# Kernel optimization log

Hardware: AMD Instinct MI355X
Metric: run time of the kernel (lower is better)

The kernel has to match this reference:

```python
import jax, jax.numpy as jnp
import numpy as np

N, E, IN, HID, H, G, CLS = 20000, 160000, 128, 96, 6, 512, 128
HD = H * HID  # heads * out_channels = 576
ARC_S = 30.0  # ArcFace scale (no margin at inference, no labels passed)


def _lin_params(key, fan_in, fan_out):
    k1, k2 = jax.random.split(key)
    lim = 1.0 / np.sqrt(fan_in)
    W = jax.random.uniform(k1, (fan_in, fan_out), minval=-lim, maxval=lim, dtype=jnp.float32)
    b = jax.random.uniform(k2, (fan_out,), minval=-lim, maxval=lim, dtype=jnp.float32)
    return W, b


def setup_inputs() -> dict:
    key = jax.random.key(0)
    ks = jax.random.split(key, 32)
    x = jax.random.normal(ks[0], (N, IN), dtype=jnp.float32)
    edge_index = jax.random.randint(ks[1], (2, E), 0, N, dtype=jnp.int64)
    batch = jnp.sort(jax.random.randint(ks[2], (N,), 0, G, dtype=jnp.int64))
    # conv1: IN -> HID (per-head dim HID, H heads)
    Wq1, bq1 = _lin_params(ks[3], IN, HD)
    Wk1, bk1 = _lin_params(ks[4], IN, HD)
    Wv1, bv1 = _lin_params(ks[5], IN, HD)
    Ws1, bs1 = _lin_params(ks[6], IN, HID)
    # convs 2..5 share shapes: HID -> HID, stacked on leading axis of 4
    def stack(fn_keys, fi, fo):
        Ws, bs = zip(*[_lin_params(k, fi, fo) for k in fn_keys])
        return jnp.stack(Ws), jnp.stack(bs)
    Wq_r, bq_r = stack(ks[7:11], HID, HD)
    Wk_r, bk_r = stack(ks[11:15], HID, HD)
    Wv_r, bv_r = stack(ks[15:19], HID, HD)
    Ws_r, bs_r = stack(ks[19:23], HID, HID)
    fc1_w, fc1_b = _lin_params(ks[23], HID, HID)
    fc2_w, fc2_b = _lin_params(ks[24], HID, HID)
    arc_w = jax.random.normal(ks[25], (CLS, HID), dtype=jnp.float32)
    return dict(x=x, edge_index=edge_index, batch=batch,
                Wq1=Wq1, bq1=bq1, Wk1=Wk1, bk1=bk1, Wv1=Wv1, bv1=bv1, Ws1=Ws1, bs1=bs1,
                Wq_r=Wq_r, bq_r=bq_r, Wk_r=Wk_r, bk_r=bk_r, Wv_r=Wv_r, bv_r=bv_r,
                Ws_r=Ws_r, bs_r=bs_r,
                fc1_w=fc1_w, fc1_b=fc1_b, fc2_w=fc2_w, fc2_b=fc2_b, arc_w=arc_w)


def transformer_conv(x, src, dst, Wq, bq, Wk, bk, Wv, bv, Ws, bs):
    n = x.shape[0]
    q = (x @ Wq + bq).reshape(n, H, HID)
    k = (x @ Wk + bk).reshape(n, H, HID)
    v = (x @ Wv + bv).reshape(n, H, HID)
    # edge-wise attention logits [E, H]
    alpha = jnp.einsum('ehd,ehd->eh', q[dst], k[src]) / jnp.sqrt(jnp.float32(HID))
    # segment softmax over incoming edges of each destination node
    m = jax.ops.segment_max(alpha, dst, num_segments=n)
    a = jnp.exp(alpha - m[dst])
    s = jax.ops.segment_sum(a, dst, num_segments=n)
    a = a / s[dst]
    out = jax.ops.segment_sum(a[:, :, None] * v[src], dst, num_segments=n)  # [n, H, HID]
    # concat=False -> mean over heads; root_weight skip connection
    return out.mean(axis=1) + x @ Ws + bs


def reference(x, edge_index, batch,
              Wq1, bq1, Wk1, bk1, Wv1, bv1, Ws1, bs1,
              Wq_r, bq_r, Wk_r, bk_r, Wv_r, bv_r, Ws_r, bs_r,
              fc1_w, fc1_b, fc2_w, fc2_b, arc_w):
    src, dst = edge_index[0], edge_index[1]
    h = jax.nn.relu(transformer_conv(x, src, dst, Wq1, bq1, Wk1, bk1, Wv1, bv1, Ws1, bs1))
    for i in range(4):  # gtconv2..gtconv5
        h = jax.nn.relu(transformer_conv(h, src, dst, Wq_r[i], bq_r[i], Wk_r[i], bk_r[i],
                                         Wv_r[i], bv_r[i], Ws_r[i], bs_r[i]))
    # global mean pool over graphs
    sums = jax.ops.segment_sum(h, batch, num_segments=G)
    cnt = jax.ops.segment_sum(jnp.ones((h.shape[0], 1), h.dtype), batch, num_segments=G)
    g = sums / jnp.maximum(cnt, 1.0)
    g = jax.nn.relu(g @ fc1_w + fc1_b)
    g = jax.nn.relu(g @ fc2_w + fc2_b)
    # ArcFace without labels: scaled cosine logits
    gn = g / (jnp.linalg.norm(g, axis=-1, keepdims=True) + 1e-12)
    wn = arc_w / (jnp.linalg.norm(arc_w, axis=-1, keepdims=True) + 1e-12)
    return ARC_S * (gn @ wn.T)
```

## Files before the change

kernel.cpp:

```cpp
#include <hip/hip_runtime.h>
#include <math.h>

#define N_NODES 20000
#define N_EDGES 160000
#define DIM_IN  128
#define HIDDEN  96
#define NH      6
#define HD      576
#define LDROW   704
#define KVF8LD  1152
#define NALL    1824
#define NGRAPH  512
#define NCLS    128
#define CHUNK   32
#define SLD     104
#define BSTR    112

typedef unsigned short ushort_t;
typedef unsigned char uchar_t;
typedef __attribute__((ext_vector_type(8))) short bf16x8;
typedef __attribute__((ext_vector_type(4))) float f32x4;
typedef __attribute__((ext_vector_type(2))) float f32x2;

static __device__ __forceinline__ ushort_t f2bf(float f) {
    unsigned int u = __float_as_uint(f);
    return (ushort_t)((u + 0x7fffu + ((u >> 16) & 1u)) >> 16);
}
static __device__ __forceinline__ float bfs(ushort_t u) { return __uint_as_float((unsigned int)u << 16); }
static __device__ __forceinline__ float bflo(unsigned int u) { return __uint_as_float(u << 16); }
static __device__ __forceinline__ float bfhi(unsigned int u) { return __uint_as_float(u & 0xffff0000u); }

__global__ void k_cvt(const float* __restrict__ src, ushort_t* __restrict__ dst, int n)
{
    int i = blockIdx.x * blockDim.x + threadIdx.x;
    if (i < n) dst[i] = f2bf(src[i]);
}

__global__ void k_cvt_wT_all(
    const float* __restrict__ Wq1, const float* __restrict__ Wk1,
    const float* __restrict__ Wv1, const float* __restrict__ Ws1,
    const float* __restrict__ Wq_r, const float* __restrict__ Wk_r,
    const float* __restrict__ Wv_r, const float* __restrict__ Ws_r,
    ushort_t* __restrict__ Wb0, ushort_t* __restrict__ Wbr)
{
    const int L = blockIdx.y;
    const int K = (L == 0) ? DIM_IN : HIDDEN;
    int i = blockIdx.x * blockDim.x + threadIdx.x;
    if (i >= K * NALL) return;
    const float *Wq, *Wk, *Wv, *Ws; ushort_t* dst;
    if (L == 0) { Wq = Wq1; Wk = Wk1; Wv = Wv1; Ws = Ws1; dst = Wb0; }
    else {
        int j = L - 1;
        Wq = Wq_r + (size_t)j * HIDDEN * HD; Wk = Wk_r + (size_t)j * HIDDEN * HD;
        Wv = Wv_r + (size_t)j * HIDDEN * HD; Ws = Ws_r + (size_t)j * HIDDEN * HIDDEN;
        dst = Wbr + (size_t)j * HIDDEN * NALL;
    }
    int n = i / K, k = i - n * K;
    float v;
    if (n < 576)       v = Wq[(size_t)k * HD + n];
    else if (n < 1152) v = Wk[(size_t)k * HD + (n - 576)];
    else if (n < 1728) v = Wv[(size_t)k * HD + (n - 1152)];
    else               v = Ws[(size_t)k * HIDDEN + (n - 1728)];
    dst[i] = f2bf(v);
}

template<int KDIM>
__global__ __launch_bounds__(256) void gemm_qkvs_mfma(
    const ushort_t* __restrict__ A, int M,
    const ushort_t* __restrict__ WbT,
    const float* __restrict__ bq, const float* __restrict__ bk,
    const float* __restrict__ bv, const float* __restrict__ bs,
    ushort_t* __restrict__ kvqs, uchar_t* __restrict__ kvf8)
{
    constexpr int LDB = KDIM + 8;
    constexpr int K8  = KDIM >> 3;
    __shared__ __align__(16) ushort_t smem[128 * SLD];
    const int t    = threadIdx.x;
    const int lane = t & 63;
    const int w    = t >> 6;
    const int wm   = w & 1, wn = w >> 1;
    const int quad = lane >> 4;
    const int l16  = lane & 15;
    const int m0   = blockIdx.y * 128;
    const int rb   = blockIdx.x;
    const int n0   = rb * 96;

    for (int idx = t; idx < 96 * K8; idx += 256) {
        int c = idx / K8, kc = idx - c * K8;
        uint4 v = *(const uint4*)(WbT + (size_t)(n0 + c) * KDIM + kc * 8);
        *(uint4*)(&smem[c * LDB + kc * 8]) = v;
    }

    const ushort_t* Arow[4];
    #pragma unroll
    for (int i = 0; i < 4; i++) {
        int row = m0 + wm * 64 + i * 16 + l16;
        row = min(row, M - 1);
        Arow[i] = A + (size_t)row * KDIM + quad * 8;
    }
    __syncthreads();

    f32x4 acc[4][3] = {};
    #pragma unroll
    for (int ks = 0; ks < KDIM; ks += 32) {
        bf16x8 af[4], bfv[3];
        #pragma unroll
        for (int i = 0; i < 4; i++) af[i] = *(const bf16x8*)(Arow[i] + ks);
        #pragma unroll
        for (int j = 0; j < 3; j++)
            bfv[j] = *(const bf16x8*)(&smem[(wn * 48 + j * 16 + l16) * LDB + ks + quad * 8]);
        #pragma unroll
        for (int i = 0; i < 4; i++)
            #pragma unroll
            for (int j = 0; j < 3; j++)
                acc[i][j] = __builtin_amdgcn_mfma_f32_16x16x32_bf16(af[i], bfv[j], acc[i][j], 0, 0, 0);
    }

    int region; const float* biasp;
    if (rb < 6)       { region = 0; biasp = bq; }
    else if (rb < 12) { region = 1; biasp = bk; }
    else if (rb < 18) { region = 2; biasp = bv; }
    else              { region = 3; biasp = bs; }
    const int colbase = (region == 3) ? 0 : (rb - region * 6) * 96;
    float bj[3];
    #pragma unroll
    for (int j = 0; j < 3; j++) bj[j] = biasp[colbase + wn * 48 + j * 16 + l16];

    __syncthreads();

    if (region == 1 || region == 2) {
        uchar_t* bstage = (uchar_t*)smem;
        #pragma unroll
        for (int i = 0; i < 4; i++) {
            #pragma unroll
            for (int r = 0; r < 4; r++) {
                int row = wm * 64 + i * 16 + quad * 4 + r;
                #pragma unroll
                for (int j = 0; j < 3; j++) {
                    float v = acc[i][j][r] + bj[j];
                    int pk = __builtin_amdgcn_cvt_pk_fp8_f32(v, v, 0, false);
                    bstage[row * BSTR + wn * 48 + j * 16 + l16] = (uchar_t)(pk & 0xff);
                }
            }
        }
        __syncthreads();
        const int c0 = (rb - 6) * 96;
        for (int idx = t; idx < 128 * 6; idx += 256) {
            int r = idx / 6, v4 = idx - r * 6;
            int row = m0 + r;
            if (row < M)
                *(uint4*)(kvf8 + (size_t)row * KVF8LD + c0 + v4 * 16) =
                    *(const uint4*)(bstage + r * BSTR + v4 * 16);
        }
    } else {
        int dstoff = (region == 0) ? n0 : 576;
        #pragma unroll
        for (int i = 0; i < 4; i++) {
            #pragma unroll
            for (int r = 0; r < 4; r++) {
                int row = wm * 64 + i * 16 + quad * 4 + r;
                #pragma unroll
                for (int j = 0; j < 3; j++)
                    smem[row * SLD + wn * 48 + j * 16 + l16] = f2bf(acc[i][j][r] + bj[j]);
            }
        }
        __syncthreads();
        for (int idx = t; idx < 128 * 12; idx += 256) {
            int r = idx / 12, v = idx - r * 12;
            int row = m0 + r;
            if (row < M)
                *(uint4*)(kvqs + (size_t)row * LDROW + dstoff + v * 8) =
                    *(const uint4*)(&smem[r * SLD + v * 8]);
        }
    }
}

__global__ void k_deg(const int* __restrict__ edst, int* __restrict__ deg)
{
    int e = blockIdx.x * blockDim.x + threadIdx.x;
    if (e < N_EDGES) atomicAdd(&deg[edst[e]], 1);
}

__global__ __launch_bounds__(1024) void k_scan(const int* __restrict__ deg,
                                               int* __restrict__ row_ptr,
                                               int* __restrict__ cursor)
{
    __shared__ int part[1024];
    int t = threadIdx.x;
    const int chunk = (N_NODES + 1023) / 1024;
    int b = t * chunk;
    int s = 0;
    for (int i = 0; i < chunk; i++)
        if (b + i < N_NODES) s += deg[b + i];
    part[t] = s;
    __syncthreads();
    for (int o = 1; o < 1024; o <<= 1) {
        int v = (t >= o) ? part[t - o] : 0;
        __syncthreads();
        part[t] += v;
        __syncthreads();
    }
    int run = part[t] - s;
    for (int i = 0; i < chunk; i++) {
        if (b + i < N_NODES) {
            row_ptr[b + i] = run;
            cursor[b + i]  = run;
            run += deg[b + i];
        }
    }
    if (t == 1023) row_ptr[N_NODES] = part[1023];
}

__global__ void k_scatter(const int* __restrict__ esrc, const int* __restrict__ edst,
                          int* __restrict__ cursor, int* __restrict__ csrc)
{
    int e = blockIdx.x * blockDim.x + threadIdx.x;
    if (e < N_EDGES) {
        int pos = atomicAdd(&cursor[edst[e]], 1);
        csrc[pos] = esrc[e];
    }
}

__global__ void k_gbound(const int* __restrict__ batch, int* __restrict__ gbound)
{
    int g = blockIdx.x * blockDim.x + threadIdx.x;
    if (g > NGRAPH) return;
    int lo = 0, hi = N_NODES;
    while (lo < hi) {
        int mid = (lo + hi) >> 1;
        if (batch[mid] < g) lo = mid + 1; else hi = mid;
    }
    gbound[g] = lo;
}

__global__ __launch_bounds__(192) void node_attn(
    const ushort_t* __restrict__ kvqs, const uchar_t* __restrict__ kvf8,
    const int* __restrict__ row_ptr, const int* __restrict__ csrc,
    ushort_t* __restrict__ hb, float* __restrict__ hf)
{
    const int n = blockIdx.x;
    const int t = threadIdx.x;
    const int lane = t & 31;
    const int g = t >> 5;
    const int el = lane >> 2;
    const int qr = lane & 3;

    __shared__ float Qs[HD];
    __shared__ float wbuf[CHUNK * NH];
    __shared__ int   srcs[CHUNK];
    __shared__ float m[NH], l[NH], scale[NH], linv[NH];
    __shared__ float arr[HD];

    const int beg = row_ptr[n], end = row_ptr[n + 1];
    const ushort_t* qk = kvqs + (size_t)n * LDROW;

    if (t < 72) {
        uint4 v = *(const uint4*)(qk + t * 8);
        unsigned int uu[4] = {v.x, v.y, v.z, v.w};
        #pragma unroll
        for (int j = 0; j < 4; j++) {
            Qs[t * 8 + 2 * j]     = bflo(uu[j]);
            Qs[t * 8 + 2 * j + 1] = bfhi(uu[j]);
        }
    }
    if (t < NH) { m[t] = -1e30f; l[t] = 0.f; }

    const int d4 = 4 * t;
    const int hh = d4 / HIDDEN;
    float a[4] = {0.f, 0.f, 0.f, 0.f};
    const float qa = 0.10206207261596577f;
    const uchar_t* vbase = kvf8 + 576 + d4;

    for (int cb = beg; cb < end; cb += CHUNK) {
        const int c = min(CHUNK, end - cb);
        __syncthreads();
        if (t < c) srcs[t] = csrc[cb + t];
        __syncthreads();

        for (int eb = 0; eb < c; eb += 8) {
            int e8 = eb + el;
            bool act = e8 < c;
            int src = srcs[act ? e8 : 0];
            const uchar_t* kp = kvf8 + (size_t)src * KVF8LD + g * HIDDEN + qr * 24;
            uint2 a0 = *(const uint2*)(kp);
            uint2 a1 = *(const uint2*)(kp + 8);
            uint2 a2 = *(const uint2*)(kp + 16);
            const float* qb = &Qs[g * HIDDEN + qr * 24];
            unsigned int uu[6] = {a0.x, a0.y, a1.x, a1.y, a2.x, a2.y};
            float p = 0.f;
            #pragma unroll
            for (int k2 = 0; k2 < 6; k2++) {
                f32x2 lo = __builtin_amdgcn_cvt_pk_f32_fp8(uu[k2], false);
                f32x2 hi = __builtin_amdgcn_cvt_pk_f32_fp8(uu[k2], true);
                p += lo[0] * qb[4 * k2]     + lo[1] * qb[4 * k2 + 1]
                   + hi[0] * qb[4 * k2 + 2] + hi[1] * qb[4 * k2 + 3];
            }
            p += __shfl_xor(p, 1, 32);
            p += __shfl_xor(p, 2, 32);
            if (act && qr == 0) wbuf[e8 * NH + g] = p * qa;
        }
        __syncthreads();

        {
            float logit = (lane < c) ? wbuf[lane * NH + g] : -1e30f;
            float cm = logit;
            #pragma unroll
            for (int o = 16; o; o >>= 1) cm = fmaxf(cm, __shfl_xor(cm, o, 32));
            cm = fmaxf(cm, m[g]);
            float wv = (lane < c) ? __expf(logit - cm) : 0.f;
            if (lane < c) wbuf[lane * NH + g] = wv;
            float lp = wv;
            #pragma unroll
            for (int o = 16; o; o >>= 1) lp += __shfl_xor(lp, o, 32);
            if (lane == 0) {
                float sc = __expf(m[g] - cm);
                scale[g] = sc;
                l[g] = l[g] * sc + lp;
                m[g] = cm;
            }
        }
        __syncthreads();

        if (t < 144) {
            float sc = scale[hh];
            #pragma unroll
            for (int j = 0; j < 4; j++) a[j] *= sc;
            int e = 0;
            for (; e + 4 <= c; e += 4) {
                unsigned int r[4];
                #pragma unroll
                for (int j = 0; j < 4; j++)
                    r[j] = *(const unsigned int*)(vbase + (size_t)srcs[e + j] * KVF8LD);
                #pragma unroll
                for (int j = 0; j < 4; j++) {
                    float w2 = wbuf[(e + j) * NH + hh];
                    f32x2 lo = __builtin_amdgcn_cvt_pk_f32_fp8(r[j], false);
                    f32x2 hi = __builtin_amdgcn_cvt_pk_f32_fp8(r[j], true);
                    a[0] += w2 * lo[0];
                    a[1] += w2 * lo[1];
                    a[2] += w2 * hi[0];
                    a[3] += w2 * hi[1];
                }
            }
            for (; e < c; e++) {
                unsigned int r = *(const unsigned int*)(vbase + (size_t)srcs[e] * KVF8LD);
                float w2 = wbuf[e * NH + hh];
                f32x2 lo = __builtin_amdgcn_cvt_pk_f32_fp8(r, false);
                f32x2 hi = __builtin_amdgcn_cvt_pk_f32_fp8(r, true);
                a[0] += w2 * lo[0];
                a[1] += w2 * lo[1];
                a[2] += w2 * hi[0];
                a[3] += w2 * hi[1];
            }
        }
    }

    if (t < NH) linv[t] = (l[t] > 0.f) ? 1.0f / l[t] : 0.f;
    __syncthreads();
    if (t < 144) {
        float li = linv[hh];
        #pragma unroll
        for (int j = 0; j < 4; j++) arr[d4 + j] = a[j] * li;
    }
    __syncthreads();

    if (t < HIDDEN) {
        float s = (arr[t] + arr[HIDDEN + t] + arr[2 * HIDDEN + t] +
                   arr[3 * HIDDEN + t] + arr[4 * HIDDEN + t] + arr[5 * HIDDEN + t])
                  * (1.0f / 6.0f);
        s += bfs(qk[576 + t]);
        s = fmaxf(s, 0.0f);
        hb[n * HIDDEN + t] = f2bf(s);
        hf[n * HIDDEN + t] = s;
    }
}

__global__ __launch_bounds__(128) void k_head(
    const float* __restrict__ hf, const int* __restrict__ gbound,
    const float* __restrict__ fc1w, const float* __restrict__ fc1b,
    const float* __restrict__ fc2w, const float* __restrict__ fc2b,
    const float* __restrict__ arcw, float* __restrict__ out)
{
    int g = blockIdx.x, t = threadIdx.x;
    __shared__ float v0[HIDDEN], v1[HIDDEN], v2[HIDDEN];
    __shared__ float gnorm;
    const int s0 = gbound[g], s1 = gbound[g + 1];
    float cnt = fmaxf((float)(s1 - s0), 1.0f);
    if (t < HIDDEN) {
        float s = 0.f;
        for (int n = s0; n < s1; n++) s += hf[(size_t)n * HIDDEN + t];
        v0[t] = s / cnt;
    }
    __syncthreads();
    if (t < HIDDEN) {
        float s = fc1b[t];
        for (int k = 0; k < HIDDEN; k++) s += v0[k] * fc1w[k * HIDDEN + t];
        v1[t] = fmaxf(s, 0.f);
    }
    __syncthreads();
    if (t < HIDDEN) {
        float s = fc2b[t];
        for (int k = 0; k < HIDDEN; k++) s += v1[k] * fc2w[k * HIDDEN + t];
        v2[t] = fmaxf(s, 0.f);
    }
    __syncthreads();
    if (t == 0) {
        float s = 0.f;
        for (int k = 0; k < HIDDEN; k++) s += v2[k] * v2[k];
        gnorm = sqrtf(s) + 1e-12f;
    }
    __syncthreads();
    if (t < NCLS) {
        float dot = 0.f, wn = 0.f;
        const float* wr = arcw + (size_t)t * HIDDEN;
        for (int k = 0; k < HIDDEN; k++) {
            float w = wr[k];
            dot += w * v2[k];
            wn  += w * w;
        }
        out[g * NCLS + t] = 30.0f * dot / (gnorm * (sqrtf(wn) + 1e-12f));
    }
}

extern "C" void kernel_launch(void* const* d_in, const int* in_sizes, int n_in,
                              void* d_out, int out_size, void* d_ws, size_t ws_size,
                              hipStream_t stream)
{
    (void)in_sizes; (void)n_in; (void)out_size; (void)ws_size;

    const float* x     = (const float*)d_in[0];
    const int*   ei    = (const int*)d_in[1];
    const int*   batch = (const int*)d_in[2];
    const float* Wq1 = (const float*)d_in[3];  const float* bq1 = (const float*)d_in[4];
    const float* Wk1 = (const float*)d_in[5];  const float* bk1 = (const float*)d_in[6];
    const float* Wv1 = (const float*)d_in[7];  const float* bv1 = (const float*)d_in[8];
    const float* Ws1 = (const float*)d_in[9];  const float* bs1 = (const float*)d_in[10];
    const float* Wq_r = (const float*)d_in[11]; const float* bq_r = (const float*)d_in[12];
    const float* Wk_r = (const float*)d_in[13]; const float* bk_r = (const float*)d_in[14];
    const float* Wv_r = (const float*)d_in[15]; const float* bv_r = (const float*)d_in[16];
    const float* Ws_r = (const float*)d_in[17]; const float* bs_r = (const float*)d_in[18];
    const float* fc1w = (const float*)d_in[19]; const float* fc1b = (const float*)d_in[20];
    const float* fc2w = (const float*)d_in[21]; const float* fc2b = (const float*)d_in[22];
    const float* arcw = (const float*)d_in[23];
    float* out = (float*)d_out;

    const int* esrc = ei;
    const int* edst = ei + N_EDGES;

    char* base = (char*)d_ws;
    size_t off = 0;
    auto alloc = [&](size_t bytes) -> void* {
        off = (off + 255) & ~(size_t)255;
        void* p = base + off;
        off += bytes;
        return p;
    };
    ushort_t* kvqs = (ushort_t*)alloc((size_t)N_NODES * LDROW * 2);
    uchar_t*  kvf8 = (uchar_t*)alloc((size_t)N_NODES * KVF8LD);
    ushort_t* xb  = (ushort_t*)alloc((size_t)N_NODES * DIM_IN * 2);
    ushort_t* hb0 = (ushort_t*)alloc((size_t)N_NODES * HIDDEN * 2);
    ushort_t* hb1 = (ushort_t*)alloc((size_t)N_NODES * HIDDEN * 2);
    float*    hf  = (float*)alloc((size_t)N_NODES * HIDDEN * 4);
    ushort_t* Wb0 = (ushort_t*)alloc((size_t)DIM_IN * NALL * 2);
    ushort_t* Wbr = (ushort_t*)alloc((size_t)4 * HIDDEN * NALL * 2);
    int*   deg     = (int*)alloc(N_NODES * 4);
    int*   row_ptr = (int*)alloc((N_NODES + 1) * 4);
    int*   cursor  = (int*)alloc(N_NODES * 4);
    int*   csrc    = (int*)alloc(N_EDGES * 4);
    int*   gbound  = (int*)alloc((NGRAPH + 1) * 4);

    k_cvt<<<(N_NODES * DIM_IN + 255) / 256, 256, 0, stream>>>(x, xb, N_NODES * DIM_IN);
    {
        dim3 gw((DIM_IN * NALL + 255) / 256, 5);
        k_cvt_wT_all<<<gw, 256, 0, stream>>>(Wq1, Wk1, Wv1, Ws1,
                                             Wq_r, Wk_r, Wv_r, Ws_r, Wb0, Wbr);
    }

    hipMemsetAsync(deg, 0, N_NODES * 4, stream);
    k_deg<<<(N_EDGES + 255) / 256, 256, 0, stream>>>(edst, deg);
    k_scan<<<1, 1024, 0, stream>>>(deg, row_ptr, cursor);
    k_scatter<<<(N_EDGES + 255) / 256, 256, 0, stream>>>(esrc, edst, cursor, csrc);
    k_gbound<<<(NGRAPH + 1 + 255) / 256, 256, 0, stream>>>(batch, gbound);

    const ushort_t* Ain = xb;
    ushort_t* hbcur = hb0;
    for (int L = 0; L < 5; L++) {
        const ushort_t* Wb = (L == 0) ? Wb0 : (Wbr + (size_t)(L - 1) * HIDDEN * NALL);
        const float *bq, *bk, *bv, *bs;
        if (L == 0) { bq = bq1; bk = bk1; bv = bv1; bs = bs1; }
        else {
            int i = L - 1;
            bq = bq_r + (size_t)i * HD; bk = bk_r + (size_t)i * HD;
            bv = bv_r + (size_t)i * HD; bs = bs_r + (size_t)i * HIDDEN;
        }
        dim3 g(19, (N_NODES + 127) / 128);
        if (L == 0)
            gemm_qkvs_mfma<DIM_IN><<<g, 256, 0, stream>>>(Ain, N_NODES, Wb,
                                                          bq, bk, bv, bs, kvqs, kvf8);
        else
            gemm_qkvs_mfma<HIDDEN><<<g, 256, 0, stream>>>(Ain, N_NODES, Wb,
                                                          bq, bk, bv, bs, kvqs, kvf8);
        node_attn<<<N_NODES, 192, 0, stream>>>(kvqs, kvf8, row_ptr, csrc, hbcur, hf);
        Ain = hbcur;
        hbcur = (hbcur == hb0) ? hb1 : hb0;
    }

    k_head<<<NGRAPH, 128, 0, stream>>>(hf, gbound, fc1w, fc1b, fc2w, fc2b, arcw, out);
}
```

Measured before the change: 530.7 us.

## Enlarge QKVS GEMM M-tile to 256 rows and merge prep kernels

The QKVS GEMM now has each warp cover 64 rows by all 96 columns, which doubles the block's M-tile to 256 rows and halves the grid. Each B fragment is reused across more rows, and the epilogue is written out in two halves through the same shared buffer. Separately, the x conversion, degree count and graph-boundary search are merged into one launch to cut launch overhead. The cost is twice the accumulator registers per thread, which may lower occupancy, and fewer blocks across the GPU.

```diff
diff --git a/kernel.cpp b/kernel.cpp
--- a/kernel.cpp
+++ b/kernel.cpp
@@ -30,10 +30,31 @@
 static __device__ __forceinline__ float bflo(unsigned int u) { return __uint_as_float(u << 16); }
 static __device__ __forceinline__ float bfhi(unsigned int u) { return __uint_as_float(u & 0xffff0000u); }
 
-__global__ void k_cvt(const float* __restrict__ src, ushort_t* __restrict__ dst, int n)
-{
-    int i = blockIdx.x * blockDim.x + threadIdx.x;
-    if (i < n) dst[i] = f2bf(src[i]);
+#define PREP_CVT_BLOCKS 10000
+#define PREP_DEG_BLOCKS 625
+#define PREP_GB_BLOCKS  3
+__global__ void k_prep(const float* __restrict__ x, ushort_t* __restrict__ xb,
+                       const int* __restrict__ edst, int* __restrict__ deg,
+                       const int* __restrict__ batch, int* __restrict__ gbound)
+{
+    int b = blockIdx.x;
+    if (b < PREP_CVT_BLOCKS) {
+        int i = b * 256 + threadIdx.x;
+        if (i < N_NODES * DIM_IN) xb[i] = f2bf(x[i]);
+    } else if (b < PREP_CVT_BLOCKS + PREP_DEG_BLOCKS) {
+        int e = (b - PREP_CVT_BLOCKS) * 256 + threadIdx.x;
+        if (e < N_EDGES) atomicAdd(&deg[edst[e]], 1);
+    } else {
+        int g = (b - PREP_CVT_BLOCKS - PREP_DEG_BLOCKS) * 256 + threadIdx.x;
+        if (g <= NGRAPH) {
+            int lo = 0, hi = N_NODES;
+            while (lo < hi) {
+                int mid = (lo + hi) >> 1;
+                if (batch[mid] < g) lo = mid + 1; else hi = mid;
+            }
+            gbound[g] = lo;
+        }
+    }
 }
 
 __global__ void k_cvt_wT_all(
@@ -78,10 +99,9 @@
     const int t    = threadIdx.x;
     const int lane = t & 63;
     const int w    = t >> 6;
-    const int wm   = w & 1, wn = w >> 1;
     const int quad = lane >> 4;
     const int l16  = lane & 15;
-    const int m0   = blockIdx.y * 128;
+    const int m0   = blockIdx.y * 256;
     const int rb   = blockIdx.x;
     const int n0   = rb * 96;
 
@@ -94,25 +114,25 @@
     const ushort_t* Arow[4];
     #pragma unroll
     for (int i = 0; i < 4; i++) {
-        int row = m0 + wm * 64 + i * 16 + l16;
+        int row = m0 + w * 64 + i * 16 + l16;
         row = min(row, M - 1);
         Arow[i] = A + (size_t)row * KDIM + quad * 8;
     }
     __syncthreads();
 
-    f32x4 acc[4][3] = {};
+    f32x4 acc[4][6] = {};
     #pragma unroll
     for (int ks = 0; ks < KDIM; ks += 32) {
-        bf16x8 af[4], bfv[3];
+        bf16x8 af[4], bfv[6];
         #pragma unroll
         for (int i = 0; i < 4; i++) af[i] = *(const bf16x8*)(Arow[i] + ks);
         #pragma unroll
-        for (int j = 0; j < 3; j++)
-            bfv[j] = *(const bf16x8*)(&smem[(wn * 48 + j * 16 + l16) * LDB + ks + quad * 8]);
+        for (int j = 0; j < 6; j++)
+            bfv[j] = *(const bf16x8*)(&smem[(j * 16 + l16) * LDB + ks + quad * 8]);
         #pragma unroll
         for (int i = 0; i < 4; i++)
             #pragma unroll
-            for (int j = 0; j < 3; j++)
+            for (int j = 0; j < 6; j++)
                 acc[i][j] = __builtin_amdgcn_mfma_f32_16x16x32_bf16(af[i], bfv[j], acc[i][j], 0, 0, 0);
     }
 
@@ -122,63 +142,67 @@
     else if (rb < 18) { region = 2; biasp = bv; }
     else              { region = 3; biasp = bs; }
     const int colbase = (region == 3) ? 0 : (rb - region * 6) * 96;
-    float bj[3];
+    float bj[6];
     #pragma unroll
-    for (int j = 0; j < 3; j++) bj[j] = biasp[colbase + wn * 48 + j * 16 + l16];
-
-    __syncthreads();
-
-    if (region == 1 || region == 2) {
-        uchar_t* bstage = (uchar_t*)smem;
-        #pragma unroll
-        for (int i = 0; i < 4; i++) {
-            #pragma unroll
-            for (int r = 0; r < 4; r++) {
-                int row = wm * 64 + i * 16 + quad * 4 + r;
+    for (int j = 0; j < 6; j++) bj[j] = biasp[colbase + j * 16 + l16];
+
+    __syncthreads();
+
+    #pragma unroll
+    for (int half = 0; half < 2; half++) {
+        if ((w >> 1) == half) {
+            int lr0 = (w & 1) * 64;
+            if (region == 1 || region == 2) {
+                uchar_t* bstage = (uchar_t*)smem;
                 #pragma unroll
-                for (int j = 0; j < 3; j++) {
-                    float v = acc[i][j][r] + bj[j];
-                    int pk = __builtin_amdgcn_cvt_pk_fp8_f32(v, v, 0, false);
-                    bstage[row * BSTR + wn * 48 + j * 16 + l16] = (uchar_t)(pk & 0xff);
+                for (int i = 0; i < 4; i++) {
+                    #pragma unroll
+                    for (int r = 0; r < 4; r++) {
+                        int row = lr0 + i * 16 + quad * 4 + r;
+                        #pragma unroll
+                        for (int j = 0; j < 6; j++) {
+                            float v = acc[i][j][r] + bj[j];
+                            int pk = __builtin_amdgcn_cvt_pk_fp8_f32(v, v, 0, false);
+                            bstage[row * BSTR + j * 16 + l16] = (uchar_t)(pk & 0xff);
+                        }
+                    }
                 }
-            }
-        }
-        __syncthreads();
-        const int c0 = (rb - 6) * 96;
-        for (int idx = t; idx < 128 * 6; idx += 256) {
-            int r = idx / 6, v4 = idx - r * 6;
-            int row = m0 + r;
-            if (row < M)
-                *(uint4*)(kvf8 + (size_t)row * KVF8LD + c0 + v4 * 16) =
-                    *(const uint4*)(bstage + r * BSTR + v4 * 16);
-        }
-    } else {
-        int dstoff = (region == 0) ? n0 : 576;
-        #pragma unroll
-        for (int i = 0; i < 4; i++) {
-            #pragma unroll
-            for (int r = 0; r < 4; r++) {
-                int row = wm * 64 + i * 16 + quad * 4 + r;
+            } else {
                 #pragma unroll
-                for (int j = 0; j < 3; j++)
-                    smem[row * SLD + wn * 48 + j * 16 + l16] = f2bf(acc[i][j][r] + bj[j]);
-            }
-        }
-        __syncthreads();
-        for (int idx = t; idx < 128 * 12; idx += 256) {
-            int r = idx / 12, v = idx - r * 12;
-            int row = m0 + r;
-            if (row < M)
-                *(uint4*)(kvqs + (size_t)row * LDROW + dstoff + v * 8) =
-                    *(const uint4*)(&smem[r * SLD + v * 8]);
-        }
-    }
-}
-
-__global__ void k_deg(const int* __restrict__ edst, int* __restrict__ deg)
-{
-    int e = blockIdx.x * blockDim.x + threadIdx.x;
-    if (e < N_EDGES) atomicAdd(&deg[edst[e]], 1);
+                for (int i = 0; i < 4; i++) {
+                    #pragma unroll
+                    for (int r = 0; r < 4; r++) {
+                        int row = lr0 + i * 16 + quad * 4 + r;
+                        #pragma unroll
+                        for (int j = 0; j < 6; j++)
+                            smem[row * SLD + j * 16 + l16] = f2bf(acc[i][j][r] + bj[j]);
+                    }
+                }
+            }
+        }
+        __syncthreads();
+        if (region == 1 || region == 2) {
+            const uchar_t* bstage = (const uchar_t*)smem;
+            const int c0 = (rb - 6) * 96;
+            for (int idx = t; idx < 128 * 6; idx += 256) {
+                int r = idx / 6, v4 = idx - r * 6;
+                int row = m0 + half * 128 + r;
+                if (row < M)
+                    *(uint4*)(kvf8 + (size_t)row * KVF8LD + c0 + v4 * 16) =
+                        *(const uint4*)(bstage + r * BSTR + v4 * 16);
+            }
+        } else {
+            int dstoff = (region == 0) ? n0 : 576;
+            for (int idx = t; idx < 128 * 12; idx += 256) {
+                int r = idx / 12, v = idx - r * 12;
+                int row = m0 + half * 128 + r;
+                if (row < M)
+                    *(uint4*)(kvqs + (size_t)row * LDROW + dstoff + v * 8) =
+                        *(const uint4*)(&smem[r * SLD + v * 8]);
+            }
+        }
+        __syncthreads();
+    }
 }
 
 __global__ __launch_bounds__(1024) void k_scan(const int* __restrict__ deg,
@@ -219,18 +243,6 @@
         int pos = atomicAdd(&cursor[edst[e]], 1);
         csrc[pos] = esrc[e];
     }
-}
-
-__global__ void k_gbound(const int* __restrict__ batch, int* __restrict__ gbound)
-{
-    int g = blockIdx.x * blockDim.x + threadIdx.x;
-    if (g > NGRAPH) return;
-    int lo = 0, hi = N_NODES;
-    while (lo < hi) {
-        int mid = (lo + hi) >> 1;
-        if (batch[mid] < g) lo = mid + 1; else hi = mid;
-    }
-    gbound[g] = lo;
 }
 
 __global__ __launch_bounds__(192) void node_attn(
@@ -469,18 +481,16 @@
     int*   csrc    = (int*)alloc(N_EDGES * 4);
     int*   gbound  = (int*)alloc((NGRAPH + 1) * 4);
 
-    k_cvt<<<(N_NODES * DIM_IN + 255) / 256, 256, 0, stream>>>(x, xb, N_NODES * DIM_IN);
+    hipMemsetAsync(deg, 0, N_NODES * 4, stream);
+    k_prep<<<PREP_CVT_BLOCKS + PREP_DEG_BLOCKS + PREP_GB_BLOCKS, 256, 0, stream>>>(
+        x, xb, edst, deg, batch, gbound);
     {
         dim3 gw((DIM_IN * NALL + 255) / 256, 5);
         k_cvt_wT_all<<<gw, 256, 0, stream>>>(Wq1, Wk1, Wv1, Ws1,
                                              Wq_r, Wk_r, Wv_r, Ws_r, Wb0, Wbr);
     }
-
-    hipMemsetAsync(deg, 0, N_NODES * 4, stream);
-    k_deg<<<(N_EDGES + 255) / 256, 256, 0, stream>>>(edst, deg);
     k_scan<<<1, 1024, 0, stream>>>(deg, row_ptr, cursor);
     k_scatter<<<(N_EDGES + 255) / 256, 256, 0, stream>>>(esrc, edst, cursor, csrc);
-    k_gbound<<<(NGRAPH + 1 + 255) / 256, 256, 0, stream>>>(batch, gbound);
 
     const ushort_t* Ain = xb;
     ushort_t* hbcur = hb0;
@@ -493,7 +503,7 @@
             bq = bq_r + (size_t)i * HD; bk = bk_r + (size_t)i * HD;
             bv = bv_r + (size_t)i * HD; bs = bs_r + (size_t)i * HIDDEN;
         }
-        dim3 g(19, (N_NODES + 127) / 128);
+        dim3 g(19, (N_NODES + 255) / 256);
         if (L == 0)
             gemm_qkvs_mfma<DIM_IN><<<g, 256, 0, stream>>>(Ain, N_NODES, Wb,
                                                           bq, bk, bv, bs, kvqs, kvf8);
```

Result: slower. 544.8 us (+2.7%).
